# Kernel optimization log

Measured on AMD Instinct MI355X. Metric: run time of the kernel, lower is better.

Reference implementation:

```python
import jax, jax.numpy as jnp
import numpy as np

ORDER = 4


def setup_inputs() -> dict:
    key = jax.random.key(0)
    k1, k2, k3, k4 = jax.random.split(key, 4)
    B, IN, OUT = 8192, 1024, 1024
    x = jax.random.normal(k1, (B, IN), dtype=jnp.float32)
    base_weight = jax.random.normal(k2, (OUT, IN), dtype=jnp.float32) * (1.0 / np.sqrt(IN))
    std = 1.0 / (IN * np.sqrt(ORDER))
    taylor_coeffs = jax.random.normal(k3, (OUT, IN, ORDER), dtype=jnp.float32) * std
    bound = 1.0 / np.sqrt(IN)
    bias = jax.random.uniform(k4, (OUT,), dtype=jnp.float32, minval=-bound, maxval=bound)
    return {"x": x, "base_weight": base_weight, "taylor_coeffs": taylor_coeffs, "bias": bias}


def reference(x, base_weight, taylor_coeffs, bias):
    # base path: SiLU(x) @ W^T
    base_out = jnp.einsum('bi,oi->bo', jax.nn.silu(x), base_weight)
    # taylor path: x_powers[b,i,k] = x**k, k=0..ORDER-1; contract with coeffs[o,i,k]
    powers = jnp.arange(ORDER, dtype=x.dtype)  # [K]
    x_powers = x[:, :, None] ** powers  # [B, IN, K]
    taylor_out = jnp.einsum('bik,oik->bo', x_powers, taylor_coeffs)
    return base_out + taylor_out + bias
```

## Files before the change

### kernel.cpp

```cpp
#include <hip/hip_runtime.h>
#include <hip/hip_bf16.h>

#define GLOBAL_AS __attribute__((address_space(1)))
#define LDS_AS    __attribute__((address_space(3)))

typedef __bf16 bf16x8 __attribute__((ext_vector_type(8)));
typedef float  f32x4  __attribute__((ext_vector_type(4)));

constexpr int BATCH = 8192;
constexpr int IN    = 1024;
constexpr int OUT   = 1024;
constexpr int KDIM  = IN * 4;
constexpr int TM = 128, TN = 128, BK = 32;

__device__ __forceinline__ unsigned short f2bf(float f) {
    union { float f; unsigned u; } v; v.f = f;
    unsigned r = v.u + 0x7fffu + ((v.u >> 16) & 1u);
    return (unsigned short)(r >> 16);
}
__device__ __forceinline__ unsigned pk(unsigned short a, unsigned short b) {
    return (unsigned)a | ((unsigned)b << 16);
}

__global__ void prep_a(const float* __restrict__ x, unsigned short* __restrict__ A) {
    int idx = blockIdx.x * 256 + threadIdx.x;
    float4 v = reinterpret_cast<const float4*>(x)[idx];
    float e0[4] = {v.x, v.y, v.z, v.w};
    unsigned short o[16];
#pragma unroll
    for (int j = 0; j < 4; ++j) {
        float xv = e0[j];
        float s  = xv / (1.0f + __expf(-xv));
        float x2 = xv * xv;
        o[4*j+0] = f2bf(s);
        o[4*j+1] = f2bf(xv);
        o[4*j+2] = f2bf(x2);
        o[4*j+3] = f2bf(x2 * xv);
    }
    uint4 d0 = make_uint4(pk(o[0],o[1]),  pk(o[2],o[3]),   pk(o[4],o[5]),   pk(o[6],o[7]));
    uint4 d1 = make_uint4(pk(o[8],o[9]),  pk(o[10],o[11]), pk(o[12],o[13]), pk(o[14],o[15]));
    uint4* dst = reinterpret_cast<uint4*>(A) + (size_t)idx * 2;
    dst[0] = d0;
    dst[1] = d1;
}

__global__ __launch_bounds__(256) void prep_w(const float* __restrict__ W,
                                              const float* __restrict__ C,
                                              const float* __restrict__ bias,
                                              unsigned short* __restrict__ Bb,
                                              float* __restrict__ be) {
    const int o = blockIdx.x, t = threadIdx.x;
    const int i0 = t * 4;
    const float4* c4 = reinterpret_cast<const float4*>(C + ((size_t)o * IN + i0) * 4);
    float4 w4 = *reinterpret_cast<const float4*>(W + (size_t)o * IN + i0);
    float wv[4] = {w4.x, w4.y, w4.z, w4.w};
    float s = 0.f;
    unsigned d[8];
#pragma unroll
    for (int j = 0; j < 4; ++j) {
        float4 c = c4[j];
        s += c.x;
        d[2*j]   = pk(f2bf(wv[j]), f2bf(c.y));
        d[2*j+1] = pk(f2bf(c.z),   f2bf(c.w));
    }
    uint4* dst = reinterpret_cast<uint4*>(Bb + (size_t)o * KDIM + i0 * 4);
    dst[0] = make_uint4(d[0], d[1], d[2], d[3]);
    dst[1] = make_uint4(d[4], d[5], d[6], d[7]);
#pragma unroll
    for (int off = 32; off > 0; off >>= 1) s += __shfl_down(s, off, 64);
    __shared__ float red[4];
    if ((t & 63) == 0) red[t >> 6] = s;
    __syncthreads();
    if (t == 0) be[o] = bias[o] + red[0] + red[1] + red[2] + red[3];
}

__global__ __launch_bounds__(256) void gemm_kan(
        const unsigned short* __restrict__ Ab,
        const unsigned short* __restrict__ Bb,
        const float* __restrict__ be,
        float* __restrict__ out) {
    __shared__ unsigned short sA[TM * BK];
    __shared__ unsigned short sB[TN * BK];

    const int t   = threadIdx.x;
    const int l   = blockIdx.x;
    const int bm  = (l & 7) * 8 + ((l >> 3) & 7);
    const int bn  = l >> 6;
    const int lane = t & 63;
    const int wave = t >> 6;
    const int wr   = wave >> 1;
    const int wc   = wave & 1;
    const int l15  = lane & 15;
    const int quad = lane >> 4;

    const int rowS = t >> 2;
    const int gsw  = (t & 3) ^ ((t >> 3) & 3);
    const int colS = gsw * 8;

    const unsigned short* pa0 = Ab + (size_t)(bm * TM + rowS) * KDIM + colS;
    const unsigned short* pa1 = pa0 + (size_t)64 * KDIM;
    const unsigned short* pb0 = Bb + (size_t)(bn * TN + rowS) * KDIM + colS;
    const unsigned short* pb1 = pb0 + (size_t)64 * KDIM;

    f32x4 acc[4][4];
    const f32x4 zero = {0.f, 0.f, 0.f, 0.f};
#pragma unroll
    for (int i = 0; i < 4; ++i)
#pragma unroll
        for (int j = 0; j < 4; ++j) acc[i][j] = zero;

    const int xq   = (quad ^ ((l15 >> 1) & 3)) * 8;
    const int aoff = (wr * 64 + l15) * BK + xq;
    const int boff = (wc * 64 + l15) * BK + xq;

    for (int k0 = 0; k0 < KDIM; k0 += BK) {
        __syncthreads();
        __builtin_amdgcn_global_load_lds((const GLOBAL_AS void*)(pa0 + k0),
                                         (LDS_AS void*)(sA + t * 8), 16, 0, 0);
        __builtin_amdgcn_global_load_lds((const GLOBAL_AS void*)(pa1 + k0),
                                         (LDS_AS void*)(sA + 2048 + t * 8), 16, 0, 0);
        __builtin_amdgcn_global_load_lds((const GLOBAL_AS void*)(pb0 + k0),
                                         (LDS_AS void*)(sB + t * 8), 16, 0, 0);
        __builtin_amdgcn_global_load_lds((const GLOBAL_AS void*)(pb1 + k0),
                                         (LDS_AS void*)(sB + 2048 + t * 8), 16, 0, 0);
        __syncthreads();

        bf16x8 af[4], bv[4];
#pragma unroll
        for (int i = 0; i < 4; ++i)
            af[i] = *reinterpret_cast<const bf16x8*>(sA + aoff + i * 16 * BK);
#pragma unroll
        for (int i = 0; i < 4; ++i)
            bv[i] = *reinterpret_cast<const bf16x8*>(sB + boff + i * 16 * BK);

#pragma unroll
        for (int mi = 0; mi < 4; ++mi)
#pragma unroll
            for (int ni = 0; ni < 4; ++ni)
                acc[mi][ni] = __builtin_amdgcn_mfma_f32_16x16x32_bf16(
                    af[mi], bv[ni], acc[mi][ni], 0, 0, 0);
    }

    float bev[4];
#pragma unroll
    for (int ni = 0; ni < 4; ++ni)
        bev[ni] = be[bn * TN + wc * 64 + ni * 16 + l15];

#pragma unroll
    for (int mi = 0; mi < 4; ++mi) {
        const int grow = bm * TM + wr * 64 + mi * 16 + quad * 4;
#pragma unroll
        for (int ni = 0; ni < 4; ++ni) {
            const int gcol = bn * TN + wc * 64 + ni * 16 + l15;
            float* po = out + (size_t)grow * OUT + gcol;
#pragma unroll
            for (int r = 0; r < 4; ++r)
                po[(size_t)r * OUT] = acc[mi][ni][r] + bev[ni];
        }
    }
}

extern "C" void kernel_launch(void* const* d_in, const int* in_sizes, int n_in,
                              void* d_out, int out_size, void* d_ws, size_t ws_size,
                              hipStream_t stream) {
    const float* x    = (const float*)d_in[0];
    const float* W    = (const float*)d_in[1];
    const float* C    = (const float*)d_in[2];
    const float* bias = (const float*)d_in[3];
    float* out = (float*)d_out;

    unsigned short* Ab = (unsigned short*)d_ws;
    unsigned short* Bb = Ab + (size_t)BATCH * KDIM;
    float*          be = (float*)(Bb + (size_t)OUT * KDIM);

    prep_a<<<dim3(BATCH * IN / 4 / 256), dim3(256), 0, stream>>>(x, Ab);
    prep_w<<<dim3(OUT), dim3(256), 0, stream>>>(W, C, bias, Bb, be);

    gemm_kan<<<dim3(512), dim3(256), 0, stream>>>(Ab, Bb, be, out);
}
```

Before: 190.8 us.

## Double-buffer GEMM K tiles with BK=64 and merge prep kernels

The GEMM now uses two LDS buffers per operand with a K tile of 64. The next tile's global-to-LDS loads are issued before computing on the current one, which leaves a single barrier per iteration and overlaps memory latency with MFMA work. The XOR swizzle is reworked for the 8-chunk rows, and launch bounds now request two blocks per CU. The two prep kernels are merged into one launch to save a launch gap, at the cost of doubled LDS use and correctness that depends on the barrier-implied wait for the async LDS loads.

```diff
diff --git a/kernel.cpp b/kernel.cpp
--- a/kernel.cpp
+++ b/kernel.cpp
@@ -11,7 +11,8 @@
 constexpr int IN    = 1024;
 constexpr int OUT   = 1024;
 constexpr int KDIM  = IN * 4;
-constexpr int TM = 128, TN = 128, BK = 32;
+constexpr int TM = 128, TN = 128, BK = 64;
+constexpr int NKT = KDIM / BK;
 
 __device__ __forceinline__ unsigned short f2bf(float f) {
     union { float f; unsigned u; } v; v.f = f;
@@ -22,65 +23,67 @@
     return (unsigned)a | ((unsigned)b << 16);
 }
 
-__global__ void prep_a(const float* __restrict__ x, unsigned short* __restrict__ A) {
-    int idx = blockIdx.x * 256 + threadIdx.x;
-    float4 v = reinterpret_cast<const float4*>(x)[idx];
-    float e0[4] = {v.x, v.y, v.z, v.w};
-    unsigned short o[16];
+__global__ __launch_bounds__(256) void prep(const float* __restrict__ x,
+                                            const float* __restrict__ W,
+                                            const float* __restrict__ C,
+                                            const float* __restrict__ bias,
+                                            unsigned short* __restrict__ Ab,
+                                            unsigned short* __restrict__ Bb,
+                                            float* __restrict__ be) {
+    if (blockIdx.x < 8192) {
+        int idx = blockIdx.x * 256 + threadIdx.x;
+        float4 v = reinterpret_cast<const float4*>(x)[idx];
+        float e0[4] = {v.x, v.y, v.z, v.w};
+        unsigned short o[16];
 #pragma unroll
-    for (int j = 0; j < 4; ++j) {
-        float xv = e0[j];
-        float s  = xv / (1.0f + __expf(-xv));
-        float x2 = xv * xv;
-        o[4*j+0] = f2bf(s);
-        o[4*j+1] = f2bf(xv);
-        o[4*j+2] = f2bf(x2);
-        o[4*j+3] = f2bf(x2 * xv);
+        for (int j = 0; j < 4; ++j) {
+            float xv = e0[j];
+            float s  = xv / (1.0f + __expf(-xv));
+            float x2 = xv * xv;
+            o[4*j+0] = f2bf(s);
+            o[4*j+1] = f2bf(xv);
+            o[4*j+2] = f2bf(x2);
+            o[4*j+3] = f2bf(x2 * xv);
+        }
+        uint4 d0 = make_uint4(pk(o[0],o[1]), pk(o[2],o[3]),   pk(o[4],o[5]),   pk(o[6],o[7]));
+        uint4 d1 = make_uint4(pk(o[8],o[9]), pk(o[10],o[11]), pk(o[12],o[13]), pk(o[14],o[15]));
+        uint4* dst = reinterpret_cast<uint4*>(Ab) + (size_t)idx * 2;
+        dst[0] = d0;
+        dst[1] = d1;
+    } else {
+        const int o = blockIdx.x - 8192, t = threadIdx.x;
+        const int i0 = t * 4;
+        const float4* c4 = reinterpret_cast<const float4*>(C + ((size_t)o * IN + i0) * 4);
+        float4 w4 = *reinterpret_cast<const float4*>(W + (size_t)o * IN + i0);
+        float wv[4] = {w4.x, w4.y, w4.z, w4.w};
+        float s = 0.f;
+        unsigned d[8];
+#pragma unroll
+        for (int j = 0; j < 4; ++j) {
+            float4 c = c4[j];
+            s += c.x;
+            d[2*j]   = pk(f2bf(wv[j]), f2bf(c.y));
+            d[2*j+1] = pk(f2bf(c.z),   f2bf(c.w));
+        }
+        uint4* dst = reinterpret_cast<uint4*>(Bb + (size_t)o * KDIM + i0 * 4);
+        dst[0] = make_uint4(d[0], d[1], d[2], d[3]);
+        dst[1] = make_uint4(d[4], d[5], d[6], d[7]);
+#pragma unroll
+        for (int off = 32; off > 0; off >>= 1) s += __shfl_down(s, off, 64);
+        __shared__ float red[4];
+        if ((t & 63) == 0) red[t >> 6] = s;
+        __syncthreads();
+        if (t == 0) be[o] = bias[o] + red[0] + red[1] + red[2] + red[3];
     }
-    uint4 d0 = make_uint4(pk(o[0],o[1]),  pk(o[2],o[3]),   pk(o[4],o[5]),   pk(o[6],o[7]));
-    uint4 d1 = make_uint4(pk(o[8],o[9]),  pk(o[10],o[11]), pk(o[12],o[13]), pk(o[14],o[15]));
-    uint4* dst = reinterpret_cast<uint4*>(A) + (size_t)idx * 2;
-    dst[0] = d0;
-    dst[1] = d1;
 }
 
-__global__ __launch_bounds__(256) void prep_w(const float* __restrict__ W,
-                                              const float* __restrict__ C,
-                                              const float* __restrict__ bias,
-                                              unsigned short* __restrict__ Bb,
-                                              float* __restrict__ be) {
-    const int o = blockIdx.x, t = threadIdx.x;
-    const int i0 = t * 4;
-    const float4* c4 = reinterpret_cast<const float4*>(C + ((size_t)o * IN + i0) * 4);
-    float4 w4 = *reinterpret_cast<const float4*>(W + (size_t)o * IN + i0);
-    float wv[4] = {w4.x, w4.y, w4.z, w4.w};
-    float s = 0.f;
-    unsigned d[8];
-#pragma unroll
-    for (int j = 0; j < 4; ++j) {
-        float4 c = c4[j];
-        s += c.x;
-        d[2*j]   = pk(f2bf(wv[j]), f2bf(c.y));
-        d[2*j+1] = pk(f2bf(c.z),   f2bf(c.w));
-    }
-    uint4* dst = reinterpret_cast<uint4*>(Bb + (size_t)o * KDIM + i0 * 4);
-    dst[0] = make_uint4(d[0], d[1], d[2], d[3]);
-    dst[1] = make_uint4(d[4], d[5], d[6], d[7]);
-#pragma unroll
-    for (int off = 32; off > 0; off >>= 1) s += __shfl_down(s, off, 64);
-    __shared__ float red[4];
-    if ((t & 63) == 0) red[t >> 6] = s;
-    __syncthreads();
-    if (t == 0) be[o] = bias[o] + red[0] + red[1] + red[2] + red[3];
-}
-
-__global__ __launch_bounds__(256) void gemm_kan(
+__global__ __launch_bounds__(256, 2) void gemm_kan(
         const unsigned short* __restrict__ Ab,
         const unsigned short* __restrict__ Bb,
         const float* __restrict__ be,
         float* __restrict__ out) {
-    __shared__ unsigned short sA[TM * BK];
-    __shared__ unsigned short sB[TN * BK];
+    __shared__ unsigned short sA[2][TM * BK];
+    __shared__ unsigned short sB[2][TN * BK];
 
     const int t   = threadIdx.x;
     const int l   = blockIdx.x;
@@ -93,14 +96,15 @@
     const int l15  = lane & 15;
     const int quad = lane >> 4;
 
-    const int rowS = t >> 2;
-    const int gsw  = (t & 3) ^ ((t >> 3) & 3);
-    const int colS = gsw * 8;
-
-    const unsigned short* pa0 = Ab + (size_t)(bm * TM + rowS) * KDIM + colS;
-    const unsigned short* pa1 = pa0 + (size_t)64 * KDIM;
-    const unsigned short* pb0 = Bb + (size_t)(bn * TN + rowS) * KDIM + colS;
-    const unsigned short* pb1 = pb0 + (size_t)64 * KDIM;
+    const int rowT = t >> 3;
+    const int gT   = (t & 7) ^ (rowT & 7);
+    const unsigned short* pa[4];
+    const unsigned short* pb[4];
+#pragma unroll
+    for (int i = 0; i < 4; ++i) {
+        pa[i] = Ab + (size_t)(bm * TM + i * 32 + rowT) * KDIM + gT * 8;
+        pb[i] = Bb + (size_t)(bn * TN + i * 32 + rowT) * KDIM + gT * 8;
+    }
 
     f32x4 acc[4][4];
     const f32x4 zero = {0.f, 0.f, 0.f, 0.f};
@@ -109,36 +113,52 @@
 #pragma unroll
         for (int j = 0; j < 4; ++j) acc[i][j] = zero;
 
-    const int xq   = (quad ^ ((l15 >> 1) & 3)) * 8;
-    const int aoff = (wr * 64 + l15) * BK + xq;
-    const int boff = (wc * 64 + l15) * BK + xq;
+    const int xr = l15 & 7;
 
-    for (int k0 = 0; k0 < KDIM; k0 += BK) {
-        __syncthreads();
-        __builtin_amdgcn_global_load_lds((const GLOBAL_AS void*)(pa0 + k0),
-                                         (LDS_AS void*)(sA + t * 8), 16, 0, 0);
-        __builtin_amdgcn_global_load_lds((const GLOBAL_AS void*)(pa1 + k0),
-                                         (LDS_AS void*)(sA + 2048 + t * 8), 16, 0, 0);
-        __builtin_amdgcn_global_load_lds((const GLOBAL_AS void*)(pb0 + k0),
-                                         (LDS_AS void*)(sB + t * 8), 16, 0, 0);
-        __builtin_amdgcn_global_load_lds((const GLOBAL_AS void*)(pb1 + k0),
-                                         (LDS_AS void*)(sB + 2048 + t * 8), 16, 0, 0);
+#pragma unroll
+    for (int i = 0; i < 4; ++i) {
+        __builtin_amdgcn_global_load_lds((const GLOBAL_AS void*)pa[i],
+                                         (LDS_AS void*)(sA[0] + i * 2048 + t * 8), 16, 0, 0);
+        __builtin_amdgcn_global_load_lds((const GLOBAL_AS void*)pb[i],
+                                         (LDS_AS void*)(sB[0] + i * 2048 + t * 8), 16, 0, 0);
+    }
+
+    for (int kt = 0; kt < NKT; ++kt) {
         __syncthreads();
 
-        bf16x8 af[4], bv[4];
+        if (kt + 1 < NKT) {
+            const int koff = (kt + 1) * BK;
+            const int nb = (kt + 1) & 1;
 #pragma unroll
-        for (int i = 0; i < 4; ++i)
-            af[i] = *reinterpret_cast<const bf16x8*>(sA + aoff + i * 16 * BK);
+            for (int i = 0; i < 4; ++i) {
+                __builtin_amdgcn_global_load_lds((const GLOBAL_AS void*)(pa[i] + koff),
+                                                 (LDS_AS void*)(sA[nb] + i * 2048 + t * 8), 16, 0, 0);
+                __builtin_amdgcn_global_load_lds((const GLOBAL_AS void*)(pb[i] + koff),
+                                                 (LDS_AS void*)(sB[nb] + i * 2048 + t * 8), 16, 0, 0);
+            }
+        }
+
+        const unsigned short* a_base = sA[kt & 1];
+        const unsigned short* b_base = sB[kt & 1];
 #pragma unroll
-        for (int i = 0; i < 4; ++i)
-            bv[i] = *reinterpret_cast<const bf16x8*>(sB + boff + i * 16 * BK);
-
+        for (int kk = 0; kk < 2; ++kk) {
+            const int cq = ((kk * 4 + quad) ^ xr) * 8;
+            bf16x8 af[4], bv[4];
 #pragma unroll
-        for (int mi = 0; mi < 4; ++mi)
+            for (int mi = 0; mi < 4; ++mi)
+                af[mi] = *reinterpret_cast<const bf16x8*>(
+                    a_base + (wr * 64 + mi * 16 + l15) * BK + cq);
 #pragma unroll
             for (int ni = 0; ni < 4; ++ni)
-                acc[mi][ni] = __builtin_amdgcn_mfma_f32_16x16x32_bf16(
-                    af[mi], bv[ni], acc[mi][ni], 0, 0, 0);
+                bv[ni] = *reinterpret_cast<const bf16x8*>(
+                    b_base + (wc * 64 + ni * 16 + l15) * BK + cq);
+#pragma unroll
+            for (int mi = 0; mi < 4; ++mi)
+#pragma unroll
+                for (int ni = 0; ni < 4; ++ni)
+                    acc[mi][ni] = __builtin_amdgcn_mfma_f32_16x16x32_bf16(
+                        af[mi], bv[ni], acc[mi][ni], 0, 0, 0);
+        }
     }
 
     float bev[4];
@@ -173,8 +193,7 @@
     unsigned short* Bb = Ab + (size_t)BATCH * KDIM;
     float*          be = (float*)(Bb + (size_t)OUT * KDIM);
 
-    prep_a<<<dim3(BATCH * IN / 4 / 256), dim3(256), 0, stream>>>(x, Ab);
-    prep_w<<<dim3(OUT), dim3(256), 0, stream>>>(W, C, bias, Bb, be);
+    prep<<<dim3(8192 + 1024), dim3(256), 0, stream>>>(x, W, C, bias, Ab, Bb, be);
 
     gemm_kan<<<dim3(512), dim3(256), 0, stream>>>(Ab, Bb, be, out);
 }
```

Result: faster. 175.5 us (-8.0%).
